# Optimization experiments

Measured on AMD Instinct MI355X. Metric: run time of the kernel, lower is better.

## Reference

```python
import jax, jax.numpy as jnp
import numpy as np

B, L, D, H = 2, 1024, 1024, 16
HEAD = D // H
BUCKETS = 256
MAX_REL = 512
ATT_SPAN = BUCKETS          # pos_ebd_size = position_buckets when buckets > 0
SCALE_FACTOR = 3            # 1 (content) + 1 (c2p) + 1 (p2c)


def _log_bucket(rel, bucket_size, max_position):
    """make_log_bucket_position: signed log-bucketed relative positions."""
    sign = jnp.sign(rel).astype(jnp.float32)
    mid = bucket_size // 2
    abs_pos = jnp.where((rel < mid) & (rel > -mid), mid - 1, jnp.abs(rel)).astype(jnp.float32)
    log_pos = jnp.ceil(jnp.log(abs_pos / mid) / np.float32(np.log((max_position - 1) / mid)) * (mid - 1)) + mid
    bucket = jnp.where(abs_pos <= mid, rel.astype(jnp.float32), log_pos * sign)
    return bucket.astype(jnp.int32)


def build_relative_position(q_len, k_len):
    rel = jnp.arange(q_len, dtype=jnp.int32)[:, None] - jnp.arange(k_len, dtype=jnp.int32)[None, :]
    return _log_bucket(rel, BUCKETS, MAX_REL)  # [q_len, k_len]


def setup_inputs() -> dict:
    key = jax.random.key(0)
    ks = jax.random.split(key, 6)
    w = 0.02  # typical init scale, keeps softmax well-conditioned
    return {
        "hidden_states": jax.random.normal(ks[0], (B, L, D), jnp.float32),
        "attention_mask": jnp.ones((B, L), jnp.int32),
        "rel_embeddings": jax.random.normal(ks[1], (2 * ATT_SPAN, D), jnp.float32) * w,
        "Wq": jax.random.normal(ks[2], (D, D), jnp.float32) * w,
        "bq": jnp.zeros((D,), jnp.float32),
        "Wk": jax.random.normal(ks[3], (D, D), jnp.float32) * w,
        "bk": jnp.zeros((D,), jnp.float32),
        "Wv": jax.random.normal(ks[4], (D, D), jnp.float32) * w,
        "bv": jnp.zeros((D,), jnp.float32),
    }


def reference(hidden_states, attention_mask, rel_embeddings, Wq, bq, Wk, bk, Wv, bv):
    Bn, Ln, Dn = hidden_states.shape

    def proj(x, W, b):  # Linear with bias, torch convention y = x W^T + b
        return x @ W.T + b

    def to_heads(x):  # [.., L, D] -> [.., H, L, HEAD]
        return x.reshape(*x.shape[:-1], H, HEAD).swapaxes(-3, -2)

    q = to_heads(proj(hidden_states, Wq, bq))  # [B,H,L,d]
    k = to_heads(proj(hidden_states, Wk, bk))
    v = to_heads(proj(hidden_states, Wv, bv))

    scale = jnp.sqrt(jnp.float32(HEAD * SCALE_FACTOR))
    scores = jnp.einsum('bhqd,bhkd->bhqk', q, k) / scale

    # disentangled relative-position bias (share_att_key=True -> reuse Wq/Wk)
    rel = build_relative_position(Ln, Ln)                     # [L,L] log-bucketed
    pos_k = proj(rel_embeddings, Wk, bk).reshape(2 * ATT_SPAN, H, HEAD)
    pos_q = proj(rel_embeddings, Wq, bq).reshape(2 * ATT_SPAN, H, HEAD)

    # c2p: Q . posK, gathered at (rel + span)
    c2p_att = jnp.einsum('bhqd,phd->bhqp', q, pos_k)          # [B,H,L,2S]
    c2p_idx = jnp.clip(rel + ATT_SPAN, 0, 2 * ATT_SPAN - 1)   # [L,L]
    c2p = jnp.take_along_axis(c2p_att, jnp.broadcast_to(c2p_idx[None, None], (Bn, H, Ln, Ln)), axis=-1)

    # p2c: K . posQ gathered at (-rel + span), then transposed to [q,k]
    p2c_att = jnp.einsum('bhkd,phd->bhkp', k, pos_q)          # [B,H,L,2S]
    p2c_idx = jnp.clip(-rel + ATT_SPAN, 0, 2 * ATT_SPAN - 1)
    p2c = jnp.take_along_axis(p2c_att, jnp.broadcast_to(p2c_idx[None, None], (Bn, H, Ln, Ln)), axis=-1)
    p2c = jnp.swapaxes(p2c, -1, -2)

    scores = scores + (c2p + p2c) / scale

    bias = jnp.where(attention_mask[:, None, None, :] > 0, 0.0, -1e9).astype(scores.dtype)
    probs = jax.nn.softmax(scores + bias, axis=-1)
    ctx = jnp.einsum('bhqk,bhkd->bhqd', probs, v)
    return ctx.swapaxes(1, 2).reshape(Bn, Ln, Dn)
```

## Files before the change

### kernel.cpp

```cpp
#include <hip/hip_runtime.h>


typedef short s8v __attribute__((ext_vector_type(8)));
typedef short s4v __attribute__((ext_vector_type(4)));
typedef float f32x4 __attribute__((ext_vector_type(4)));
typedef float f4v __attribute__((ext_vector_type(4)));

#define QK_SCALE 0.26864243f

__device__ __forceinline__ unsigned short f2bf(float f) {
  unsigned u = __builtin_bit_cast(unsigned, f);
  u += 0x7fffu + ((u >> 16) & 1u);
  return (unsigned short)(u >> 16);
}
__device__ __forceinline__ float bf2f(unsigned short h) {
  unsigned u = ((unsigned)h) << 16;
  return __builtin_bit_cast(float, u);
}

__device__ __forceinline__ void gload_lds16(const void* g, void* l) {
  __builtin_amdgcn_global_load_lds(
      (const __attribute__((address_space(1))) void*)g,
      (__attribute__((address_space(3))) void*)l, 16, 0, 0);
}

__global__ __launch_bounds__(256) void prep_kernel(
    const float* __restrict__ hidden, const float* __restrict__ rel,
    const float* __restrict__ Wq, const float* __restrict__ Wk,
    const float* __restrict__ Wv, const int* __restrict__ mask,
    short* __restrict__ Abf, short* __restrict__ Wbf,
    float* __restrict__ mbias, short* __restrict__ Tt) {
  int idx = blockIdx.x * 256 + threadIdx.x;
  const int NCONV = 1441792;
  if (idx < NCONV) {
    const float* src; short* dst; int off;
    if (idx < 524288) { src = hidden; dst = Abf; off = idx; }
    else if (idx < 655360) { src = rel; dst = Abf + 2048 * 1024; off = idx - 524288; }
    else {
      int j = idx - 655360;
      int w = j / 262144; off = j - w * 262144;
      src = (w == 0) ? Wq : (w == 1) ? Wk : Wv;
      dst = Wbf + w * 1048576;
    }
    f4v v = ((const f4v*)src)[off];
    s4v o;
    o[0] = (short)f2bf(v[0]); o[1] = (short)f2bf(v[1]);
    o[2] = (short)f2bf(v[2]); o[3] = (short)f2bf(v[3]);
    ((s4v*)dst)[off] = o;
  } else {
    int j = idx - NCONV;
    if (j < 2047) {
      int r = j - 1023;
      float fr = (float)r;
      float sign = (r > 0) ? 1.f : ((r < 0) ? -1.f : 0.f);
      float abs_pos = (r < 128 && r > -128) ? 127.f : fabsf(fr);
      const float logc = 1.3843393245589053f;
      float log_pos = ceilf(logf(abs_pos * (1.f / 128.f)) / logc * 127.f) + 128.f;
      float bucket = (abs_pos <= 128.f) ? fr : log_pos * sign;
      int bi = (int)bucket + 256;
      bi = bi < 0 ? 0 : (bi > 511 ? 511 : bi);
      Tt[j] = (short)bi;
    } else if (j < 4095) {
      int m = j - 2047;
      mbias[m] = (mask[m] > 0) ? 0.f : -1e9f;
    }
  }
}

__global__ __launch_bounds__(256) void gemm_qkv(
    const short* __restrict__ Abf, const short* __restrict__ Wbf,
    const float* __restrict__ bq, const float* __restrict__ bk,
    const float* __restrict__ bv,
    short* __restrict__ Qc, short* __restrict__ Kc, short* __restrict__ Vc) {
  __shared__ short As[128 * 64];
  __shared__ short Bs[128 * 64];
  int tid = threadIdx.x;
  int wid = tid >> 6, lane = tid & 63;
  int lr = lane & 15, lg = lane >> 4;
  int wr = wid >> 1, wc = wid & 1;
  int z = blockIdx.z;
  int brow = blockIdx.y * 128;
  if (z == 2 && brow >= 2048) return;
  const short* W = Wbf + z * 1048576;
  const float* bias = (z == 0) ? bq : (z == 1) ? bk : bv;
  short* C = (z == 0) ? Qc : (z == 1) ? Kc : Vc;
  float scale = (z == 2) ? 1.f : QK_SCALE;
  int bcol = blockIdx.x * 128;

  f32x4 acc[4][4];
  for (int i = 0; i < 4; i++)
    for (int j = 0; j < 4; j++) acc[i][j] = (f32x4){0.f, 0.f, 0.f, 0.f};

  for (int k0 = 0; k0 < 1024; k0 += 64) {
    for (int i = 0; i < 4; i++) {
      int n = i * 256 + wid * 64 + lane;
      int row = n >> 3, cswz = n & 7, cb = cswz ^ (row & 7);
      const short* gA = Abf + (size_t)(brow + row) * 1024 + k0 + cb * 8;
      gload_lds16(gA, &As[(i * 256 + wid * 64) * 8]);
      const short* gB = W + (size_t)(bcol + row) * 1024 + k0 + cb * 8;
      gload_lds16(gB, &Bs[(i * 256 + wid * 64) * 8]);
    }
    __syncthreads();
    for (int ks = 0; ks < 2; ks++) {
      s8v af[4], bfv[4];
      for (int mi = 0; mi < 4; mi++) {
        int row = wr * 64 + mi * 16 + lr, cb = ks * 4 + lg;
        af[mi] = *(const s8v*)&As[row * 64 + (cb ^ (row & 7)) * 8];
      }
      for (int ni = 0; ni < 4; ni++) {
        int row = wc * 64 + ni * 16 + lr, cb = ks * 4 + lg;
        bfv[ni] = *(const s8v*)&Bs[row * 64 + (cb ^ (row & 7)) * 8];
      }
      for (int mi = 0; mi < 4; mi++)
        for (int ni = 0; ni < 4; ni++)
          acc[mi][ni] = __builtin_amdgcn_mfma_f32_16x16x32_bf16(
              af[mi], bfv[ni], acc[mi][ni], 0, 0, 0);
    }
    __syncthreads();
  }
  for (int mi = 0; mi < 4; mi++)
    for (int ni = 0; ni < 4; ni++) {
      int col = bcol + wc * 64 + ni * 16 + lr;
      float bb = bias[col];
      for (int r = 0; r < 4; r++) {
        int row = brow + wr * 64 + mi * 16 + lg * 4 + r;
        float v = (acc[mi][ni][r] + bb) * scale;
        C[(size_t)row * 1024 + col] = (short)f2bf(v);
      }
    }
}

__global__ __launch_bounds__(256) void pos_trans(
    const short* __restrict__ Qc, const short* __restrict__ Kc,
    const short* __restrict__ Vc, const float* __restrict__ mbias,
    short* __restrict__ c2p, short* __restrict__ p2c,
    short* __restrict__ Vt) {
  __shared__ short sh[2 * 128 * 64];
  int tid = threadIdx.x;
  if (blockIdx.z < 64) {
    short* As = sh;
    short* Bs = sh + 128 * 64;
    int wid = tid >> 6, lane = tid & 63;
    int lr = lane & 15, lg = lane >> 4;
    int wr = wid >> 1, wc = wid & 1;
    int zz = blockIdx.z;
    int which = zz >> 5;
    int bh = zz & 31;
    int b = bh >> 4, h = bh & 15;
    const short* Arows = (which == 0) ? Qc : Kc;
    const short* Brows = (which == 0) ? Kc : Qc;
    short* Out = (which == 0) ? c2p : p2c;
    int mrow = blockIdx.y * 128;
    int ncol = blockIdx.x * 128;

    for (int i = 0; i < 4; i++) {
      int n = i * 256 + wid * 64 + lane;
      const short* gA = Arows + (size_t)(b * 1024 + mrow + (n >> 3)) * 1024 + h * 64 + (n & 7) * 8;
      gload_lds16(gA, &As[(i * 256 + wid * 64) * 8]);
      const short* gB = Brows + (size_t)(2048 + ncol + (n >> 3)) * 1024 + h * 64 + (n & 7) * 8;
      gload_lds16(gB, &Bs[(i * 256 + wid * 64) * 8]);
    }
    __syncthreads();

    f32x4 acc[4][4];
    for (int i = 0; i < 4; i++)
      for (int j = 0; j < 4; j++) acc[i][j] = (f32x4){0.f, 0.f, 0.f, 0.f};
    for (int ks = 0; ks < 2; ks++) {
      s8v af[4], bfv[4];
      for (int mi = 0; mi < 4; mi++)
        af[mi] = *(const s8v*)&As[(wr * 64 + mi * 16 + lr) * 64 + ks * 32 + lg * 8];
      for (int ni = 0; ni < 4; ni++)
        bfv[ni] = *(const s8v*)&Bs[(wc * 64 + ni * 16 + lr) * 64 + ks * 32 + lg * 8];
      for (int mi = 0; mi < 4; mi++)
        for (int ni = 0; ni < 4; ni++)
          acc[mi][ni] = __builtin_amdgcn_mfma_f32_16x16x32_bf16(
              af[mi], bfv[ni], acc[mi][ni], 0, 0, 0);
    }
    size_t base = (size_t)(b * 16 + h) * 1024;
    for (int mi = 0; mi < 4; mi++)
      for (int ni = 0; ni < 4; ni++)
        for (int r = 0; r < 4; r++) {
          int m = mrow + wr * 64 + mi * 16 + lg * 4 + r;
          int nn = ncol + wc * 64 + ni * 16 + lr;
          float v = acc[mi][ni][r];
          if (which == 1) v += mbias[b * 1024 + m];
          Out[(base + m) * 512 + nn] = (short)f2bf(v);
        }
  } else {
    short* TL = sh;
    int idx = ((blockIdx.z - 64) * 8 + blockIdx.y) * 4 + blockIdx.x;
    int b = idx >> 8, h = (idx >> 4) & 15, lt = idx & 15;
    for (int i = 0; i < 2; i++) {
      int n = i * 256 + tid;
      int l = n >> 3, c = n & 7;
      s8v v = *(const s8v*)&Vc[(size_t)(b * 1024 + lt * 64 + l) * 1024 + h * 64 + c * 8];
      *(s8v*)&TL[l * 72 + c * 8] = v;
    }
    __syncthreads();
    for (int i = 0; i < 2; i++) {
      int m = i * 256 + tid;
      int d = m >> 3, c = m & 7;
      s8v o;
      for (int jj = 0; jj < 8; jj++) o[jj] = TL[(c * 8 + jj) * 72 + d];
      *(s8v*)&Vt[((size_t)(b * 16 + h) * 64 + d) * 1024 + lt * 64 + c * 8] = o;
    }
  }
}

__global__ __launch_bounds__(256) void bias_build(
    const short* __restrict__ c2p, const short* __restrict__ p2c,
    const short* __restrict__ Tt, short* __restrict__ bias) {
  __shared__ short Wc[64 * 66];
  __shared__ short Wp[64 * 66];
  __shared__ short Tl[128];
  int tid = threadIdx.x;
  int wid = tid >> 6, lane = tid & 63;
  int lr = lane & 15, lg = lane >> 4;
  int qt = blockIdx.x, kt = blockIdx.y, bh = blockIdx.z;
  int q0 = qt * 64, k0 = kt * 64;
  int relbase = q0 - k0;
  size_t bh1024 = (size_t)bh * 1024;

  if (tid < 127) Tl[tid] = Tt[relbase + 960 + tid];
  __syncthreads();

#pragma unroll
  for (int ii = 0; ii < 16; ii++) {
    int row = wid * 16 + ii;
    int w0 = Tl[row];
    int col = w0 + lane; col = col > 511 ? 511 : col;
    Wc[row * 66 + lane] = c2p[(bh1024 + q0 + row) * 512 + col];
    int w0p_ = Tl[63 - row];
    int colp = w0p_ + lane; colp = colp > 511 ? 511 : colp;
    Wp[row * 66 + lane] = p2c[(bh1024 + k0 + row) * 512 + colp];
  }
  __syncthreads();

  int w0c[4], w0p[4];
#pragma unroll
  for (int r = 0; r < 4; r++) w0c[r] = Tl[wid * 16 + lg * 4 + r];
#pragma unroll
  for (int n = 0; n < 4; n++) w0p[n] = Tl[63 - (n * 16 + lr)];

  s8v o0, o1;
#pragma unroll
  for (int n = 0; n < 4; n++)
#pragma unroll
    for (int r = 0; r < 4; r++) {
      int qq = wid * 16 + lg * 4 + r;
      int kk = n * 16 + lr;
      int p = Tl[qq - kk + 63];
      float v = bf2f((unsigned short)Wc[qq * 66 + p - w0c[r]]) +
                bf2f((unsigned short)Wp[kk * 66 + p - w0p[n]]);
      short s = (short)f2bf(v);
      if (n < 2) o0[(n & 1) * 4 + r] = s; else o1[(n & 1) * 4 + r] = s;
    }
  size_t tile = ((size_t)bh * 16 + qt) * 16 + kt;
  size_t base = (tile * 4 + wid) * 1024 + lane * 8;
  *(s8v*)&bias[base] = o0;
  *(s8v*)&bias[base + 512] = o1;
}

template <int NSPLIT>
__global__ __launch_bounds__(256) void attn_frag(
    const short* __restrict__ Qc, const short* __restrict__ Kc,
    const short* __restrict__ Vt, const short* __restrict__ bias,
    float* __restrict__ Opart, float* __restrict__ dpart,
    float* __restrict__ out) {
  const int KSEG = 1024 / NSPLIT;
  const int NT = KSEG / 64;
  __shared__ short Kl[2][64 * 64];
  __shared__ short Vl[2][64 * 64];
  __shared__ short Pl[4][16 * 72];
  int tid = threadIdx.x;
  int wid = tid >> 6, lane = tid & 63;
  int lr = lane & 15, lg = lane >> 4;
  int qt = blockIdx.x, h = blockIdx.y, z = blockIdx.z;
  int b = (NSPLIT == 1) ? z : (z / NSPLIT);
  int ks = (NSPLIT == 1) ? 0 : (z % NSPLIT);
  int k0seg = ks * KSEG;
  int q0 = qt * 64, qbase = q0 + wid * 16;

  s8v aq[2];
  for (int s_ = 0; s_ < 2; s_++)
    aq[s_] = *(const s8v*)&Qc[(size_t)(b * 1024 + qbase + lr) * 1024 + h * 64 + s_ * 32 + lg * 8];

  f32x4 oacc[4];
  for (int n = 0; n < 4; n++) oacc[n] = (f32x4){0.f, 0.f, 0.f, 0.f};
  float dsum[4] = {0.f, 0.f, 0.f, 0.f};

  auto stage = [&](int t, int buf) {
#pragma unroll
    for (int i = 0; i < 2; i++) {
      int n = i * 256 + tid;
      int row = n >> 3, cswz = n & 7, cb = cswz ^ (row & 7);
      gload_lds16(&Kc[(size_t)(b * 1024 + k0seg + t * 64 + row) * 1024 + h * 64 + cb * 8],
                  &Kl[buf][(i * 256 + wid * 64) * 8]);
      gload_lds16(&Vt[((size_t)(b * 16 + h) * 64 + row) * 1024 + k0seg + t * 64 + cb * 8],
                  &Vl[buf][(i * 256 + wid * 64) * 8]);
    }
  };
  auto fload = [&](int t, s8v& f0, s8v& f1) {
    size_t tile = (((size_t)(b * 16 + h) * 16 + qt) * 16 + (k0seg >> 6) + t);
    size_t base = (tile * 4 + wid) * 1024 + lane * 8;
    f0 = *(const s8v*)&bias[base];
    f1 = *(const s8v*)&bias[base + 512];
  };

  s8v fb0, fb1, fn0, fn1;
  stage(0, 0);
  fload(0, fb0, fb1);
  __syncthreads();

#pragma unroll
  for (int t = 0; t < NT; ++t) {
    const int cur = t & 1, nxt = cur ^ 1;

    if (t + 1 < NT) {
      stage(t + 1, nxt);
      fload(t + 1, fn0, fn1);
    }

    f32x4 sacc[4];
#pragma unroll
    for (int n = 0; n < 4; n++) sacc[n] = (f32x4){0.f, 0.f, 0.f, 0.f};
#pragma unroll
    for (int s_ = 0; s_ < 2; s_++)
#pragma unroll
      for (int n = 0; n < 4; n++) {
        int row = n * 16 + lr, cb = s_ * 4 + lg, cbs = cb ^ (row & 7);
        s8v bk_ = *(const s8v*)&Kl[cur][row * 64 + cbs * 8];
        sacc[n] = __builtin_amdgcn_mfma_f32_16x16x32_bf16(aq[s_], bk_, sacc[n], 0, 0, 0);
      }

#pragma unroll
    for (int n = 0; n < 4; n++)
#pragma unroll
      for (int r = 0; r < 4; r++) {
        unsigned short bv_ = (unsigned short)((n < 2 ? fb0 : fb1)[(n & 1) * 4 + r]);
        float p = __expf(sacc[n][r] + bf2f(bv_));
        dsum[r] += p;
        Pl[wid][(lg * 4 + r) * 72 + n * 16 + lr] = (short)f2bf(p);
      }
    asm volatile("s_waitcnt lgkmcnt(0)" ::: "memory");

#pragma unroll
    for (int s_ = 0; s_ < 2; s_++) {
      s8v ap = *(const s8v*)&Pl[wid][lr * 72 + s_ * 32 + lg * 8];
#pragma unroll
      for (int n = 0; n < 4; n++) {
        int row = n * 16 + lr, cb = s_ * 4 + lg, cbs = cb ^ (row & 7);
        s8v bv_ = *(const s8v*)&Vl[cur][row * 64 + cbs * 8];
        oacc[n] = __builtin_amdgcn_mfma_f32_16x16x32_bf16(ap, bv_, oacc[n], 0, 0, 0);
      }
    }

    __syncthreads();

    if (t + 1 < NT) { fb0 = fn0; fb1 = fn1; }
  }

  for (int m = 1; m < 16; m <<= 1)
    for (int r = 0; r < 4; r++) dsum[r] += __shfl_xor(dsum[r], m, 64);

  if (NSPLIT == 1) {
    for (int n = 0; n < 4; n++)
      for (int r = 0; r < 4; r++) {
        int q = qbase + lg * 4 + r;
        int d = n * 16 + lr;
        out[(size_t)(b * 1024 + q) * 1024 + h * 64 + d] = oacc[n][r] / dsum[r];
      }
  } else {
    size_t po = ((size_t)(z * 16 + h)) * 65536;
    for (int n = 0; n < 4; n++)
      for (int r = 0; r < 4; r++) {
        int q = qbase + lg * 4 + r;
        Opart[po + (size_t)q * 64 + n * 16 + lr] = oacc[n][r];
      }
    if (lr == 0)
      for (int r = 0; r < 4; r++)
        dpart[(z * 16 + h) * 1024 + qbase + lg * 4 + r] = dsum[r];
  }
}

template <int NSPLIT>
__global__ __launch_bounds__(256) void attn_gather(
    const short* __restrict__ Qc, const short* __restrict__ Kc,
    const short* __restrict__ Vt, const short* __restrict__ c2p,
    const short* __restrict__ p2c, const short* __restrict__ Tt,
    float* __restrict__ Opart, float* __restrict__ dpart,
    float* __restrict__ out) {
  const int KSEG = 1024 / NSPLIT;
  const int NT = KSEG / 64;
  const int TLN = 64 + KSEG - 1;
  __shared__ short Kl[2][64 * 64];
  __shared__ short Vl[2][64 * 64];
  __shared__ short Pl[4][16 * 72];
  __shared__ short Tl[TLN + 1];
  int tid = threadIdx.x;
  int wid = tid >> 6, lane = tid & 63;
  int lr = lane & 15, lg = lane >> 4;
  int qt = blockIdx.x, h = blockIdx.y, z = blockIdx.z;
  int b = (NSPLIT == 1) ? z : (z / NSPLIT);
  int ks = (NSPLIT == 1) ? 0 : (z % NSPLIT);
  int k0seg = ks * KSEG;
  int q0 = qt * 64, qbase = q0 + wid * 16;
  size_t bh1024 = (size_t)(b * 16 + h) * 1024;

  for (int i = tid; i < TLN; i += 256) Tl[i] = Tt[(q0 - k0seg - (KSEG - 1) + 1023) + i];

  s8v aq[2];
  for (int s_ = 0; s_ < 2; s_++)
    aq[s_] = *(const s8v*)&Qc[(size_t)(b * 1024 + qbase + lr) * 1024 + h * 64 + s_ * 32 + lg * 8];

  f32x4 oacc[4];
  for (int n = 0; n < 4; n++) oacc[n] = (f32x4){0.f, 0.f, 0.f, 0.f};
  float dsum[4] = {0.f, 0.f, 0.f, 0.f};
  __syncthreads();

  auto stage = [&](int t, int buf) {
#pragma unroll
    for (int i = 0; i < 2; i++) {
      int n = i * 256 + tid;
      int row = n >> 3, cswz = n & 7, cb = cswz ^ (row & 7);
      gload_lds16(&Kc[(size_t)(b * 1024 + k0seg + t * 64 + row) * 1024 + h * 64 + cb * 8],
                  &Kl[buf][(i * 256 + wid * 64) * 8]);
      gload_lds16(&Vt[((size_t)(b * 16 + h) * 64 + row) * 1024 + k0seg + t * 64 + cb * 8],
                  &Vl[buf][(i * 256 + wid * 64) * 8]);
    }
  };
  auto gather = [&](int t, unsigned short* cg, unsigned short* pg) {
#pragma unroll
    for (int n = 0; n < 4; n++) {
      int k = k0seg + t * 64 + n * 16 + lr;
      size_t prow = (bh1024 + k) * 512;
      int jb = wid * 16 - t * 64 - lr + (KSEG - 1) - n * 16 + lg * 4;
#pragma unroll
      for (int r = 0; r < 4; r++) {
        int q = qbase + lg * 4 + r;
        int idx = Tl[jb + r];
        cg[n * 4 + r] = (unsigned short)c2p[(bh1024 + q) * 512 + idx];
        pg[n * 4 + r] = (unsigned short)p2c[prow + idx];
      }
    }
  };

  unsigned short c2g[16], p2g[16], c2n[16], p2n[16];
  stage(0, 0);
  gather(0, c2g, p2g);
  __syncthreads();

#pragma unroll
  for (int t = 0; t < NT; ++t) {
    const int cur = t & 1, nxt = cur ^ 1;
    if (t + 1 < NT) { stage(t + 1, nxt); gather(t + 1, c2n, p2n); }

    f32x4 sacc[4];
#pragma unroll
    for (int n = 0; n < 4; n++) sacc[n] = (f32x4){0.f, 0.f, 0.f, 0.f};
#pragma unroll
    for (int s_ = 0; s_ < 2; s_++)
#pragma unroll
      for (int n = 0; n < 4; n++) {
        int row = n * 16 + lr, cb = s_ * 4 + lg, cbs = cb ^ (row & 7);
        s8v bk_ = *(const s8v*)&Kl[cur][row * 64 + cbs * 8];
        sacc[n] = __builtin_amdgcn_mfma_f32_16x16x32_bf16(aq[s_], bk_, sacc[n], 0, 0, 0);
      }
#pragma unroll
    for (int n = 0; n < 4; n++)
#pragma unroll
      for (int r = 0; r < 4; r++) {
        float bias = bf2f(c2g[n * 4 + r]) + bf2f(p2g[n * 4 + r]);
        float p = __expf(sacc[n][r] + bias);
        dsum[r] += p;
        Pl[wid][(lg * 4 + r) * 72 + n * 16 + lr] = (short)f2bf(p);
      }
    asm volatile("s_waitcnt lgkmcnt(0)" ::: "memory");
#pragma unroll
    for (int s_ = 0; s_ < 2; s_++) {
      s8v ap = *(const s8v*)&Pl[wid][lr * 72 + s_ * 32 + lg * 8];
#pragma unroll
      for (int n = 0; n < 4; n++) {
        int row = n * 16 + lr, cb = s_ * 4 + lg, cbs = cb ^ (row & 7);
        s8v bv_ = *(const s8v*)&Vl[cur][row * 64 + cbs * 8];
        oacc[n] = __builtin_amdgcn_mfma_f32_16x16x32_bf16(ap, bv_, oacc[n], 0, 0, 0);
      }
    }
    __syncthreads();
    if (t + 1 < NT) {
#pragma unroll
      for (int i = 0; i < 16; i++) { c2g[i] = c2n[i]; p2g[i] = p2n[i]; }
    }
  }

  for (int m = 1; m < 16; m <<= 1)
    for (int r = 0; r < 4; r++) dsum[r] += __shfl_xor(dsum[r], m, 64);

  if (NSPLIT == 1) {
    for (int n = 0; n < 4; n++)
      for (int r = 0; r < 4; r++) {
        int q = qbase + lg * 4 + r;
        int d = n * 16 + lr;
        out[(size_t)(b * 1024 + q) * 1024 + h * 64 + d] = oacc[n][r] / dsum[r];
      }
  } else {
    size_t po = ((size_t)(z * 16 + h)) * 65536;
    for (int n = 0; n < 4; n++)
      for (int r = 0; r < 4; r++) {
        int q = qbase + lg * 4 + r;
        Opart[po + (size_t)q * 64 + n * 16 + lr] = oacc[n][r];
      }
    if (lr == 0)
      for (int r = 0; r < 4; r++)
        dpart[(z * 16 + h) * 1024 + qbase + lg * 4 + r] = dsum[r];
  }
}

template <int NSPLIT>
__global__ __launch_bounds__(256) void combine_kernel(
    const float* __restrict__ Opart, const float* __restrict__ dpart,
    float* __restrict__ out) {
  int idx = blockIdx.x * 256 + threadIdx.x;
  int pos = idx * 4;
  int b = pos >> 20;
  int q = (pos >> 10) & 1023;
  int hd = pos & 1023;
  int h = hd >> 6, d = hd & 63;
  f4v s = (f4v){0.f, 0.f, 0.f, 0.f};
  float dn = 0.f;
  for (int ks = 0; ks < NSPLIT; ks++) {
    int zh = (b * NSPLIT + ks) * 16 + h;
    s += *(const f4v*)&Opart[(size_t)zh * 65536 + q * 64 + d];
    dn += dpart[zh * 1024 + q];
  }
  f4v r = s / dn;
  *(f4v*)&out[pos] = r;
}

extern "C" void kernel_launch(void* const* d_in, const int* in_sizes, int n_in,
                              void* d_out, int out_size, void* d_ws, size_t ws_size,
                              hipStream_t stream) {
  (void)in_sizes; (void)n_in; (void)out_size;
  const float* hidden = (const float*)d_in[0];
  const int* mask = (const int*)d_in[1];
  const float* rel = (const float*)d_in[2];
  const float* Wq = (const float*)d_in[3];
  const float* bq = (const float*)d_in[4];
  const float* Wk = (const float*)d_in[5];
  const float* bk = (const float*)d_in[6];
  const float* Wv = (const float*)d_in[7];
  const float* bv = (const float*)d_in[8];
  float* out = (float*)d_out;

  char* w = (char*)d_ws;
  short* Abf = (short*)w; w += 2560 * 1024 * 2;
  short* Wbf = (short*)w; w += 3 * 1024 * 1024 * 2;
  short* Qc  = (short*)w; w += 2560 * 1024 * 2;
  short* Kc  = (short*)w; w += 2560 * 1024 * 2;
  short* Vc  = (short*)w; w += 2560 * 1024 * 2;
  short* Vt  = (short*)w; w += 2 * 16 * 64 * 1024 * 2;
  short* c2p = (short*)w; w += (size_t)2 * 16 * 1024 * 512 * 2;
  short* p2c = (short*)w; w += (size_t)2 * 16 * 1024 * 512 * 2;
  short* Tt  = (short*)w; w += 4096;
  float* mbias = (float*)w; w += 8192;
  short* bias_frag = (short*)w;
  size_t need_frag = (size_t)(w - (char*)d_ws) + (size_t)8192 * 4096 * 2;
  float* Opart_old = (float*)w;
  size_t need_old = (size_t)(w - (char*)d_ws) + (size_t)8 * 16 * 1024 * 64 * 4 + 8 * 16 * 1024 * 4;

  prep_kernel<<<5648, 256, 0, stream>>>(hidden, rel, Wq, Wk, Wv, mask, Abf, Wbf, mbias, Tt);
  gemm_qkv<<<dim3(8, 20, 3), 256, 0, stream>>>(Abf, Wbf, bq, bk, bv, Qc, Kc, Vc);
  pos_trans<<<dim3(4, 8, 80), 256, 0, stream>>>(Qc, Kc, Vc, mbias, c2p, p2c, Vt);

  if (ws_size >= need_frag) {
    float* Opart = (float*)c2p;
    float* dpart = (float*)p2c;
    bias_build<<<dim3(16, 16, 32), 256, 0, stream>>>(c2p, p2c, Tt, bias_frag);
    attn_frag<2><<<dim3(16, 16, 4), 256, 0, stream>>>(Qc, Kc, Vt, bias_frag,
                                                      Opart, dpart, out);
    combine_kernel<2><<<2048, 256, 0, stream>>>(Opart, dpart, out);
  } else if (ws_size >= need_old) {
    float* Opart = Opart_old;
    float* dpart = (float*)((char*)Opart_old + (size_t)8 * 16 * 1024 * 64 * 4);
    attn_gather<4><<<dim3(16, 16, 8), 256, 0, stream>>>(Qc, Kc, Vt, c2p, p2c, Tt,
                                                        Opart, dpart, out);
    combine_kernel<4><<<2048, 256, 0, stream>>>(Opart, dpart, out);
  } else {
    attn_gather<1><<<dim3(16, 16, 2), 256, 0, stream>>>(Qc, Kc, Vt, c2p, p2c, Tt,
                                                        (float*)Opart_old, (float*)Opart_old, out);
  }
}
```

Baseline: 137.2 us.

## Fuse split-K combine into attention via atomic counter; swizzle pos GEMM LDS

Drops the separate combine kernel. Each attention block now bumps a per-(batch,head,qtile) atomic counter after writing its partial output, and the second split to arrive reads its partner's partial sums, adds them and writes the normalized output. The counters are reset inside bias_build. Separately, the LDS layout of the position GEMM is XOR-swizzled to avoid bank conflicts on the fragment loads. The risks are correctness if memory ordering is wrong and the extra global reads done by the last-arriving blocks.

Result: slower. 223.0 us (+62.6%).

```diff
diff --git a/kernel.cpp b/kernel.cpp
--- a/kernel.cpp
+++ b/kernel.cpp
@@ -155,9 +155,10 @@
 
     for (int i = 0; i < 4; i++) {
       int n = i * 256 + wid * 64 + lane;
-      const short* gA = Arows + (size_t)(b * 1024 + mrow + (n >> 3)) * 1024 + h * 64 + (n & 7) * 8;
+      int row = n >> 3, cswz = n & 7, cb = cswz ^ (row & 7);
+      const short* gA = Arows + (size_t)(b * 1024 + mrow + row) * 1024 + h * 64 + cb * 8;
       gload_lds16(gA, &As[(i * 256 + wid * 64) * 8]);
-      const short* gB = Brows + (size_t)(2048 + ncol + (n >> 3)) * 1024 + h * 64 + (n & 7) * 8;
+      const short* gB = Brows + (size_t)(2048 + ncol + row) * 1024 + h * 64 + cb * 8;
       gload_lds16(gB, &Bs[(i * 256 + wid * 64) * 8]);
     }
     __syncthreads();
@@ -167,10 +168,14 @@
       for (int j = 0; j < 4; j++) acc[i][j] = (f32x4){0.f, 0.f, 0.f, 0.f};
     for (int ks = 0; ks < 2; ks++) {
       s8v af[4], bfv[4];
-      for (int mi = 0; mi < 4; mi++)
-        af[mi] = *(const s8v*)&As[(wr * 64 + mi * 16 + lr) * 64 + ks * 32 + lg * 8];
-      for (int ni = 0; ni < 4; ni++)
-        bfv[ni] = *(const s8v*)&Bs[(wc * 64 + ni * 16 + lr) * 64 + ks * 32 + lg * 8];
+      for (int mi = 0; mi < 4; mi++) {
+        int row = wr * 64 + mi * 16 + lr, cb = ks * 4 + lg;
+        af[mi] = *(const s8v*)&As[row * 64 + (cb ^ (row & 7)) * 8];
+      }
+      for (int ni = 0; ni < 4; ni++) {
+        int row = wc * 64 + ni * 16 + lr, cb = ks * 4 + lg;
+        bfv[ni] = *(const s8v*)&Bs[row * 64 + (cb ^ (row & 7)) * 8];
+      }
       for (int mi = 0; mi < 4; mi++)
         for (int ni = 0; ni < 4; ni++)
           acc[mi][ni] = __builtin_amdgcn_mfma_f32_16x16x32_bf16(
@@ -209,7 +214,8 @@
 
 __global__ __launch_bounds__(256) void bias_build(
     const short* __restrict__ c2p, const short* __restrict__ p2c,
-    const short* __restrict__ Tt, short* __restrict__ bias) {
+    const short* __restrict__ Tt, short* __restrict__ bias,
+    int* __restrict__ cnt) {
   __shared__ short Wc[64 * 66];
   __shared__ short Wp[64 * 66];
   __shared__ short Tl[128];
@@ -217,6 +223,7 @@
   int wid = tid >> 6, lane = tid & 63;
   int lr = lane & 15, lg = lane >> 4;
   int qt = blockIdx.x, kt = blockIdx.y, bh = blockIdx.z;
+  if (kt == 0 && tid == 0) cnt[bh * 16 + qt] = 0;
   int q0 = qt * 64, k0 = kt * 64;
   int relbase = q0 - k0;
   size_t bh1024 = (size_t)bh * 1024;
@@ -266,7 +273,7 @@
     const short* __restrict__ Qc, const short* __restrict__ Kc,
     const short* __restrict__ Vt, const short* __restrict__ bias,
     float* __restrict__ Opart, float* __restrict__ dpart,
-    float* __restrict__ out) {
+    int* __restrict__ cnt, float* __restrict__ out) {
   const int KSEG = 1024 / NSPLIT;
   const int NT = KSEG / 64;
   __shared__ short Kl[2][64 * 64];
@@ -380,6 +387,37 @@
     if (lr == 0)
       for (int r = 0; r < 4; r++)
         dpart[(z * 16 + h) * 1024 + qbase + lg * 4 + r] = dsum[r];
+
+    __shared__ int amFinal;
+    __syncthreads();
+    if (tid == 0) {
+      __threadfence();
+      int pair = (b * 16 + h) * 16 + qt;
+      int prev = atomicAdd(&cnt[pair], 1);
+      amFinal = (prev == 1);
+    }
+    __syncthreads();
+    if (amFinal) {
+      __threadfence();
+      int zp = b * NSPLIT + (ks ^ 1);
+      size_t pp = ((size_t)(zp * 16 + h)) * 65536;
+      for (int n = 0; n < 4; n++)
+        for (int r = 0; r < 4; r++) {
+          int q = qbase + lg * 4 + r;
+          oacc[n][r] += Opart[pp + (size_t)q * 64 + n * 16 + lr];
+        }
+      float dtot[4];
+      for (int r = 0; r < 4; r++) {
+        int q = qbase + lg * 4 + r;
+        dtot[r] = dsum[r] + dpart[(zp * 16 + h) * 1024 + q];
+      }
+      for (int n = 0; n < 4; n++)
+        for (int r = 0; r < 4; r++) {
+          int q = qbase + lg * 4 + r;
+          out[(size_t)(b * 1024 + q) * 1024 + h * 64 + n * 16 + lr] =
+              oacc[n][r] / dtot[r];
+        }
+    }
   }
 }
 
@@ -564,7 +602,8 @@
   short* Tt  = (short*)w; w += 4096;
   float* mbias = (float*)w; w += 8192;
   short* bias_frag = (short*)w;
-  size_t need_frag = (size_t)(w - (char*)d_ws) + (size_t)8192 * 4096 * 2;
+  int* cnt = (int*)(w + (size_t)8192 * 4096 * 2);
+  size_t need_frag = (size_t)(w - (char*)d_ws) + (size_t)8192 * 4096 * 2 + 4096;
   float* Opart_old = (float*)w;
   size_t need_old = (size_t)(w - (char*)d_ws) + (size_t)8 * 16 * 1024 * 64 * 4 + 8 * 16 * 1024 * 4;
 
@@ -575,10 +614,9 @@
   if (ws_size >= need_frag) {
     float* Opart = (float*)c2p;
     float* dpart = (float*)p2c;
-    bias_build<<<dim3(16, 16, 32), 256, 0, stream>>>(c2p, p2c, Tt, bias_frag);
+    bias_build<<<dim3(16, 16, 32), 256, 0, stream>>>(c2p, p2c, Tt, bias_frag, cnt);
     attn_frag<2><<<dim3(16, 16, 4), 256, 0, stream>>>(Qc, Kc, Vt, bias_frag,
-                                                      Opart, dpart, out);
-    combine_kernel<2><<<2048, 256, 0, stream>>>(Opart, dpart, out);
+                                                      Opart, dpart, cnt, out);
   } else if (ws_size >= need_old) {
     float* Opart = Opart_old;
     float* dpart = (float*)((char*)Opart_old + (size_t)8 * 16 * 1024 * 64 * 4);
```
